# Optimization experiments

Measured on AMD Instinct MI355X. Metric: run time of the kernel, lower is better.

## Reference

```python
import jax, jax.numpy as jnp
import numpy as np

NUM_CLASSES = 81
NEG_RATIO = 3
POS_FRAC = 0.03  # realistic fraction of positive (matched) anchors


def setup_inputs() -> dict:
    key = jax.random.key(0)
    k1, k2, k3, k4, k5 = jax.random.split(key, 5)
    B, A, C = 64, 8732, NUM_CLASSES
    pred_loc = jax.random.normal(k1, (B, A, 4), dtype=jnp.float32)
    pred_conf = jax.random.normal(k2, (B, A, C), dtype=jnp.float32)
    gt_loc = jax.random.normal(k3, (B, A, 4), dtype=jnp.float32)
    raw_cls = jax.random.randint(k4, (B, A), 1, C)
    is_pos = jax.random.uniform(k5, (B, A)) < POS_FRAC
    gt_label = jnp.where(is_pos, raw_cls, 0).astype(jnp.int32)
    return {"pred_loc": pred_loc, "pred_conf": pred_conf, "gt_loc": gt_loc, "gt_label": gt_label}


def reference(pred_loc, pred_conf, gt_loc, gt_label):
    # pred_loc/gt_loc: [B, A, 4]; pred_conf: [B, A, C]; gt_label: [B, A] int
    pos = gt_label > 0  # [B, A]

    # Smooth L1 (beta=1), summed over positive anchors only (mask instead of boolean gather)
    d = jnp.abs(pred_loc - gt_loc)
    sl1 = jnp.where(d < 1.0, 0.5 * d * d, d - 0.5)
    loc_loss = jnp.sum(sl1 * pos[..., None].astype(sl1.dtype))

    # Per-anchor cross-entropy
    logp = jax.nn.log_softmax(pred_conf, axis=-1)  # [B, A, C]
    ce = -jnp.take_along_axis(logp, gt_label[..., None].astype(jnp.int32), axis=-1)[..., 0]  # [B, A]

    cef = ce.reshape(-1)
    posf = pos.reshape(-1)
    num_pos = jnp.sum(posf)
    num_neg = jnp.minimum(NEG_RATIO * num_pos, posf.size - num_pos)

    # Hard-negative mining: rank negatives by CE descending; select top num_neg.
    neg_vals = jnp.where(posf, -jnp.inf, cef)
    order = jnp.argsort(-neg_vals)  # indices sorted by descending negative loss
    rank = jnp.zeros_like(order).at[order].set(jnp.arange(order.size))
    neg_sel = (rank < num_neg) & (~posf)

    pos_conf_loss = jnp.sum(jnp.where(posf, cef, 0.0))
    neg_conf_loss = jnp.sum(jnp.where(neg_sel, cef, 0.0))

    total = (loc_loss + pos_conf_loss + neg_conf_loss) / num_pos.astype(cef.dtype)
    return total
```

## Files before the change

### kernel.cpp

```cpp
#include <hip/hip_runtime.h>
#include <hip/hip_bf16.h>
#include <math.h>

#define NB   64
#define NA   8732
#define NCLS 81
#define NTOT (NB * NA)
#define NTILE (NTOT / 16)
#define NSLICE 64
#define K1BLK  4096
#define SUMBLK 256

#define OFF_KEYS   0
#define OFF_HISTA  (NTOT * 4)
#define OFF_HIST2  (OFF_HISTA + NSLICE * 256 * 4)
#define OFF_SCAL   (OFF_HIST2 + 4096 * 4)
#define OFF_PBNP   (OFF_SCAL + 64)
#define OFF_PBPC   (OFF_PBNP + K1BLK * 4)
#define OFF_PBNEG  (OFF_PBPC + K1BLK * 4)
#define OFF_PBLOC  (OFF_PBNEG + SUMBLK * 4)
#define OFF_PBBIN  (OFF_PBLOC + SUMBLK * 4)
#define ZERO_BYTES (NSLICE * 256 * 4 + 4096 * 4 + 64)

__device__ __forceinline__ unsigned f2k(float f) {
  unsigned u = __float_as_uint(f);
  return (u & 0x80000000u) ? ~u : (u | 0x80000000u);
}
__device__ __forceinline__ float k2fv(unsigned u) {
  return __uint_as_float((u & 0x80000000u) ? (u ^ 0x80000000u) : ~u);
}

#define DPPF(v, ctrl) \
  __int_as_float(__builtin_amdgcn_update_dpp(0, __float_as_int(v), ctrl, 0xF, 0xF, true))

__global__ __launch_bounds__(256, 7) void mbl_k1(
    const float* __restrict__ pred_conf, const int* __restrict__ gt_label,
    unsigned* __restrict__ keys, unsigned* __restrict__ hista,
    unsigned* __restrict__ pb_np, float* __restrict__ pb_pc) {
  __shared__ float srow[4][1312];
  __shared__ unsigned lhist[256];
  __shared__ float s_pc[4];
  __shared__ unsigned s_np[4];
  lhist[threadIdx.x] = 0u;
  __syncthreads();

  const int lane = threadIdx.x & 63;
  const int wid  = threadIdx.x >> 6;
  const int gw   = (blockIdx.x << 2) + wid;
  const int l    = lane & 3;
  const int q    = lane >> 2;
  float* slice = srow[wid];
  float4* s4 = (float4*)slice;

  float posconf = 0.f;
  unsigned npos = 0u;

  for (int tile = gw; tile < NTILE; tile += K1BLK * 4) {
    const float4* src = (const float4*)pred_conf + (unsigned)tile * 324u;
    const float4 r0 = src[lane];
    const float4 r1 = src[lane + 64];
    const float4 r2 = src[lane + 128];
    const float4 r3 = src[lane + 192];
    const float4 r4 = src[lane + 256];
    float4 r5;
    if (lane < 4) r5 = src[lane + 320];
    const int lab = gt_label[(tile << 4) + q];

    s4[lane]       = r0;
    s4[lane + 64]  = r1;
    s4[lane + 128] = r2;
    s4[lane + 192] = r3;
    s4[lane + 256] = r4;
    if (lane < 4) s4[lane + 320] = r5;

    const int rb = q * 81;
    float e = 0.f;
#pragma unroll
    for (int j = 0; j < 20; ++j) e += __expf(slice[rb + l + 4 * j]);
    if (l == 0) e += __expf(slice[rb + 80]);
    e += DPPF(e, 0xB1);
    e += DPPF(e, 0x4E);
    const float pick = slice[rb + lab];

    if (l == 0) {
      const float ce = __logf(e) - pick;
      const int a = (tile << 4) + q;
      if (lab > 0) {
        npos += 1u; posconf += ce; keys[a] = 0u;
      } else {
        const unsigned u = f2k(ce);
        keys[a] = u;
        atomicAdd(&lhist[u >> 24], 1u);
      }
    }
  }

#pragma unroll
  for (int s = 1; s < 64; s <<= 1) {
    posconf += __shfl_xor(posconf, s);
    npos    += (unsigned)__shfl_xor((int)npos, s);
  }
  if ((threadIdx.x & 63) == 0) { s_pc[wid] = posconf; s_np[wid] = npos; }
  __syncthreads();
  if (threadIdx.x == 0) {
    pb_pc[blockIdx.x] = s_pc[0] + s_pc[1] + s_pc[2] + s_pc[3];
    pb_np[blockIdx.x] = s_np[0] + s_np[1] + s_np[2] + s_np[3];
  }
  const unsigned hv = lhist[threadIdx.x];
  if (hv) atomicAdd(&hista[(blockIdx.x & (NSLICE - 1)) * 256 + threadIdx.x], hv);
}

__global__ __launch_bounds__(256) void mbl_sel1(const unsigned* __restrict__ hista,
                                                const unsigned* __restrict__ pb_np,
                                                const float* __restrict__ pb_pc,
                                                unsigned* __restrict__ scal_u,
                                                float* __restrict__ scal_f) {
  __shared__ unsigned partial[256];
  __shared__ float q_pc[4];
  __shared__ unsigned q_np[4];
  __shared__ unsigned s_k;
  const int t = threadIdx.x;

  unsigned np = 0u; float pc = 0.f;
  for (int i = t; i < K1BLK; i += 256) { np += pb_np[i]; pc += pb_pc[i]; }
#pragma unroll
  for (int s = 1; s < 64; s <<= 1) {
    np += (unsigned)__shfl_xor((int)np, s);
    pc += __shfl_xor(pc, s);
  }
  if ((t & 63) == 0) { q_np[t >> 6] = np; q_pc[t >> 6] = pc; }
  __syncthreads();
  if (t == 0) {
    const unsigned tot = q_np[0] + q_np[1] + q_np[2] + q_np[3];
    scal_u[0] = tot;
    scal_f[2] = q_pc[0] + q_pc[1] + q_pc[2] + q_pc[3];
    const unsigned k = min(3u * tot, (unsigned)NTOT - tot);
    s_k = k; scal_u[4] = k;
    if (k == 0u) {
      scal_u[7] = 0xFFFFFFFFu; scal_u[8] = 0u;
      scal_u[9] = 0xFFFFFFFFu; scal_u[10] = 1u;
    }
  }
  __syncthreads();
  const unsigned k = s_k;
  if (k == 0u) return;

  unsigned s = 0u;
  for (int sl = 0; sl < NSLICE; ++sl) s += hista[sl * 256 + t];
  unsigned val = s;
  partial[t] = val;
  __syncthreads();
  for (int off = 1; off < 256; off <<= 1) {
    const unsigned add = (t + off < 256) ? partial[t + off] : 0u;
    __syncthreads();
    val += add;
    partial[t] = val;
    __syncthreads();
  }
  const unsigned suf = val - s;
  if (suf < k && k <= suf + s) { scal_u[5] = (unsigned)t; scal_u[6] = suf; }
}

__global__ __launch_bounds__(256) void mbl_h2(const unsigned* __restrict__ keys,
                                              unsigned* __restrict__ hist2,
                                              const unsigned* __restrict__ scal_u) {
  if (scal_u[4] == 0u) return;
  __shared__ unsigned lh[4096];
  for (int i = threadIdx.x; i < 4096; i += 256) lh[i] = 0u;
  __syncthreads();
  const unsigned b1 = scal_u[5];
  const int stride = gridDim.x * 256;
  for (int i = blockIdx.x * 256 + threadIdx.x; i < NTOT; i += stride) {
    const unsigned key = keys[i];
    if ((key >> 24) == b1) atomicAdd(&lh[(key >> 12) & 0xFFFu], 1u);
  }
  __syncthreads();
  for (int i = threadIdx.x; i < 4096; i += 256) {
    const unsigned v = lh[i];
    if (v) atomicAdd(&hist2[i], v);
  }
}

__global__ __launch_bounds__(1024) void mbl_sel2(const unsigned* __restrict__ hist2,
                                                 unsigned* __restrict__ scal_u) {
  __shared__ unsigned partial[1024];
  if (scal_u[4] == 0u) return;
  const unsigned kt = scal_u[4] - scal_u[6];
  const unsigned b1 = scal_u[5];
  const int t = threadIdx.x;
  unsigned s = 0u;
#pragma unroll
  for (int i = 0; i < 4; ++i) s += hist2[t * 4 + i];
  unsigned val = s;
  partial[t] = val;
  __syncthreads();
  for (int off = 1; off < 1024; off <<= 1) {
    const unsigned add = (t + off < 1024) ? partial[t + off] : 0u;
    __syncthreads();
    val += add;
    partial[t] = val;
    __syncthreads();
  }
  const unsigned suf = val - s;
  if (suf < kt && kt <= suf + s) {
    unsigned c = suf;
    for (int b = 3; b >= 0; --b) {
      const unsigned h = hist2[t * 4 + b];
      if (c + h >= kt) {
        const unsigned bin = (unsigned)(t * 4 + b);
        scal_u[7] = (b1 << 24) | (bin << 12) | 0xFFFu;
        scal_u[9] = (b1 << 12) | bin;
        scal_u[8] = kt - c;
        scal_u[10] = h;
        break;
      }
      c += h;
    }
  }
}

__global__ __launch_bounds__(256) void mbl_sum(
    const unsigned* __restrict__ keys, const int* __restrict__ gt_label,
    const float* __restrict__ pred_loc, const float* __restrict__ gt_loc,
    const unsigned* __restrict__ scal_u,
    float* __restrict__ pb_neg, float* __restrict__ pb_loc,
    float* __restrict__ pb_bin) {
  __shared__ float q_n[4], q_l[4], q_b[4];
  const unsigned T = scal_u[7];
  const unsigned P20 = scal_u[9];
  float acc = 0.f, lacc = 0.f, bacc = 0.f;
  const int stride = gridDim.x * 256;
  for (int i = blockIdx.x * 256 + threadIdx.x; i < NTOT; i += stride) {
    const unsigned key = keys[i];
    if (key > T) acc += k2fv(key);
    else if ((key >> 12) == P20) bacc += k2fv(key);
    const int lb = gt_label[i];
    if (lb > 0) {
      const float4 pl = ((const float4*)pred_loc)[i];
      const float4 gl = ((const float4*)gt_loc)[i];
      float d;
      d = fabsf(pl.x - gl.x); lacc += (d < 1.f) ? 0.5f * d * d : d - 0.5f;
      d = fabsf(pl.y - gl.y); lacc += (d < 1.f) ? 0.5f * d * d : d - 0.5f;
      d = fabsf(pl.z - gl.z); lacc += (d < 1.f) ? 0.5f * d * d : d - 0.5f;
      d = fabsf(pl.w - gl.w); lacc += (d < 1.f) ? 0.5f * d * d : d - 0.5f;
    }
  }
#pragma unroll
  for (int s = 1; s < 64; s <<= 1) {
    acc  += __shfl_xor(acc, s);
    lacc += __shfl_xor(lacc, s);
    bacc += __shfl_xor(bacc, s);
  }
  const int wv = threadIdx.x >> 6;
  if ((threadIdx.x & 63) == 0) { q_n[wv] = acc; q_l[wv] = lacc; q_b[wv] = bacc; }
  __syncthreads();
  if (threadIdx.x == 0) {
    pb_neg[blockIdx.x] = q_n[0] + q_n[1] + q_n[2] + q_n[3];
    pb_loc[blockIdx.x] = q_l[0] + q_l[1] + q_l[2] + q_l[3];
    pb_bin[blockIdx.x] = q_b[0] + q_b[1] + q_b[2] + q_b[3];
  }
}

__global__ __launch_bounds__(256) void mbl_fin(const unsigned* __restrict__ scal_u,
                                               const float* __restrict__ scal_f,
                                               const float* __restrict__ pb_neg,
                                               const float* __restrict__ pb_loc,
                                               const float* __restrict__ pb_bin,
                                               float* __restrict__ out) {
  __shared__ float q_n[4], q_l[4], q_b[4];
  const int t = threadIdx.x;
  float n = pb_neg[t], l = pb_loc[t], b = pb_bin[t];
#pragma unroll
  for (int s = 1; s < 64; s <<= 1) {
    n += __shfl_xor(n, s);
    l += __shfl_xor(l, s);
    b += __shfl_xor(b, s);
  }
  const int wv = t >> 6;
  if ((t & 63) == 0) { q_n[wv] = n; q_l[wv] = l; q_b[wv] = b; }
  __syncthreads();
  if (t == 0) {
    float negsum = q_n[0] + q_n[1] + q_n[2] + q_n[3];
    const float locsum = q_l[0] + q_l[1] + q_l[2] + q_l[3];
    const float binsum = q_b[0] + q_b[1] + q_b[2] + q_b[3];
    const unsigned r = scal_u[8];
    if (r > 0u) negsum += (float)r * (binsum / (float)scal_u[10]);
    out[0] = (locsum + scal_f[2] + negsum) / (float)scal_u[0];
  }
}

extern "C" void kernel_launch(void* const* d_in, const int* in_sizes, int n_in,
                              void* d_out, int out_size, void* d_ws, size_t ws_size,
                              hipStream_t stream) {
  const float* pred_loc  = (const float*)d_in[0];
  const float* pred_conf = (const float*)d_in[1];
  const float* gt_loc    = (const float*)d_in[2];
  const int*   gt_label  = (const int*)d_in[3];
  float* out = (float*)d_out;

  char* ws = (char*)d_ws;
  unsigned* keys   = (unsigned*)(ws + OFF_KEYS);
  unsigned* hista  = (unsigned*)(ws + OFF_HISTA);
  unsigned* hist2  = (unsigned*)(ws + OFF_HIST2);
  unsigned* scal_u = (unsigned*)(ws + OFF_SCAL);
  float*    scal_f = (float*)(ws + OFF_SCAL);
  unsigned* pb_np  = (unsigned*)(ws + OFF_PBNP);
  float*    pb_pc  = (float*)(ws + OFF_PBPC);
  float*    pb_neg = (float*)(ws + OFF_PBNEG);
  float*    pb_loc = (float*)(ws + OFF_PBLOC);
  float*    pb_bin = (float*)(ws + OFF_PBBIN);

  hipMemsetAsync(ws + OFF_HISTA, 0, ZERO_BYTES, stream);

  mbl_k1<<<K1BLK, 256, 0, stream>>>(pred_conf, gt_label, keys, hista, pb_np, pb_pc);
  mbl_sel1<<<1, 256, 0, stream>>>(hista, pb_np, pb_pc, scal_u, scal_f);
  mbl_h2<<<256, 256, 0, stream>>>(keys, hist2, scal_u);
  mbl_sel2<<<1, 1024, 0, stream>>>(hist2, scal_u);
  mbl_sum<<<SUMBLK, 256, 0, stream>>>(keys, gt_label, pred_loc, gt_loc, scal_u,
                                      pb_neg, pb_loc, pb_bin);
  mbl_fin<<<1, 256, 0, stream>>>(scal_u, scal_f, pb_neg, pb_loc, pb_bin, out);
}
```

Measured before the change: 69.98 us.

## Fuse selection stages into histogram and sum kernels to cut launches

Merges the single-block threshold selections into the kernels that follow them. Every block of the second-histogram kernel redundantly reduces the per-block counts and scans the coarse histogram. Every block of the sum kernel redundantly scans the fine histogram. The final reduction is folded in through a last-block atomic ticket. This removes three kernel launches and their serialization gaps, at the cost of redundant per-block scan work and a threadfence/atomic tail.

```diff
diff --git a/kernel.cpp b/kernel.cpp
--- a/kernel.cpp
+++ b/kernel.cpp
@@ -9,18 +9,20 @@
 #define NTILE (NTOT / 16)
 #define NSLICE 64
 #define K1BLK  4096
+#define T1BLK  256
 #define SUMBLK 256
 
 #define OFF_KEYS   0
 #define OFF_HISTA  (NTOT * 4)
 #define OFF_HIST2  (OFF_HISTA + NSLICE * 256 * 4)
 #define OFF_SCAL   (OFF_HIST2 + 4096 * 4)
-#define OFF_PBNP   (OFF_SCAL + 64)
+#define OFF_TICK   (OFF_SCAL + 64)
+#define OFF_PBNP   (OFF_TICK + 64)
 #define OFF_PBPC   (OFF_PBNP + K1BLK * 4)
 #define OFF_PBNEG  (OFF_PBPC + K1BLK * 4)
 #define OFF_PBLOC  (OFF_PBNEG + SUMBLK * 4)
 #define OFF_PBBIN  (OFF_PBLOC + SUMBLK * 4)
-#define ZERO_BYTES (NSLICE * 256 * 4 + 4096 * 4 + 64)
+#define ZERO_BYTES (NSLICE * 256 * 4 + 4096 * 4 + 64 + 64)
 
 __device__ __forceinline__ unsigned f2k(float f) {
   unsigned u = __float_as_uint(f);
@@ -110,15 +112,16 @@
   if (hv) atomicAdd(&hista[(blockIdx.x & (NSLICE - 1)) * 256 + threadIdx.x], hv);
 }
 
-__global__ __launch_bounds__(256) void mbl_sel1(const unsigned* __restrict__ hista,
-                                                const unsigned* __restrict__ pb_np,
-                                                const float* __restrict__ pb_pc,
-                                                unsigned* __restrict__ scal_u,
-                                                float* __restrict__ scal_f) {
+__global__ __launch_bounds__(256) void mbl_t1(
+    const unsigned* __restrict__ keys, const unsigned* __restrict__ hista,
+    const unsigned* __restrict__ pb_np, const float* __restrict__ pb_pc,
+    unsigned* __restrict__ hist2,
+    unsigned* __restrict__ scal_u, float* __restrict__ scal_f) {
+  __shared__ unsigned lh[4096];
   __shared__ unsigned partial[256];
   __shared__ float q_pc[4];
   __shared__ unsigned q_np[4];
-  __shared__ unsigned s_k;
+  __shared__ unsigned s_k, s_b1, s_cnt;
   const int t = threadIdx.x;
 
   unsigned np = 0u; float pc = 0.f;
@@ -132,13 +135,12 @@
   __syncthreads();
   if (t == 0) {
     const unsigned tot = q_np[0] + q_np[1] + q_np[2] + q_np[3];
-    scal_u[0] = tot;
-    scal_f[2] = q_pc[0] + q_pc[1] + q_pc[2] + q_pc[3];
     const unsigned k = min(3u * tot, (unsigned)NTOT - tot);
-    s_k = k; scal_u[4] = k;
-    if (k == 0u) {
-      scal_u[7] = 0xFFFFFFFFu; scal_u[8] = 0u;
-      scal_u[9] = 0xFFFFFFFFu; scal_u[10] = 1u;
+    s_k = k;
+    if (blockIdx.x == 0) {
+      scal_u[0] = tot;
+      scal_f[2] = q_pc[0] + q_pc[1] + q_pc[2] + q_pc[3];
+      scal_u[4] = k;
     }
   }
   __syncthreads();
@@ -158,79 +160,82 @@
     __syncthreads();
   }
   const unsigned suf = val - s;
-  if (suf < k && k <= suf + s) { scal_u[5] = (unsigned)t; scal_u[6] = suf; }
-}
-
-__global__ __launch_bounds__(256) void mbl_h2(const unsigned* __restrict__ keys,
-                                              unsigned* __restrict__ hist2,
-                                              const unsigned* __restrict__ scal_u) {
-  if (scal_u[4] == 0u) return;
-  __shared__ unsigned lh[4096];
-  for (int i = threadIdx.x; i < 4096; i += 256) lh[i] = 0u;
-  __syncthreads();
-  const unsigned b1 = scal_u[5];
+  if (suf < k && k <= suf + s) { s_b1 = (unsigned)t; s_cnt = suf; }
+  __syncthreads();
+  const unsigned b1 = s_b1;
+  if (blockIdx.x == 0 && t == 0) { scal_u[5] = b1; scal_u[6] = s_cnt; }
+
+  for (int i = t; i < 4096; i += 256) lh[i] = 0u;
+  __syncthreads();
   const int stride = gridDim.x * 256;
-  for (int i = blockIdx.x * 256 + threadIdx.x; i < NTOT; i += stride) {
+  for (int i = blockIdx.x * 256 + t; i < NTOT; i += stride) {
     const unsigned key = keys[i];
     if ((key >> 24) == b1) atomicAdd(&lh[(key >> 12) & 0xFFFu], 1u);
   }
   __syncthreads();
-  for (int i = threadIdx.x; i < 4096; i += 256) {
+  for (int i = t; i < 4096; i += 256) {
     const unsigned v = lh[i];
     if (v) atomicAdd(&hist2[i], v);
   }
 }
 
-__global__ __launch_bounds__(1024) void mbl_sel2(const unsigned* __restrict__ hist2,
-                                                 unsigned* __restrict__ scal_u) {
-  __shared__ unsigned partial[1024];
-  if (scal_u[4] == 0u) return;
-  const unsigned kt = scal_u[4] - scal_u[6];
-  const unsigned b1 = scal_u[5];
+__global__ __launch_bounds__(256) void mbl_t2(
+    const unsigned* __restrict__ keys, const int* __restrict__ gt_label,
+    const float* __restrict__ pred_loc, const float* __restrict__ gt_loc,
+    const unsigned* __restrict__ hist2,
+    const unsigned* __restrict__ scal_u, const float* __restrict__ scal_f,
+    float* __restrict__ pb_neg, float* __restrict__ pb_loc,
+    float* __restrict__ pb_bin, unsigned* __restrict__ tick,
+    float* __restrict__ out) {
+  __shared__ unsigned partial[256];
+  __shared__ float q_n[4], q_l[4], q_b[4];
+  __shared__ unsigned s_T, s_P20, s_r, s_bt;
+  __shared__ bool s_last;
   const int t = threadIdx.x;
-  unsigned s = 0u;
-#pragma unroll
-  for (int i = 0; i < 4; ++i) s += hist2[t * 4 + i];
-  unsigned val = s;
-  partial[t] = val;
-  __syncthreads();
-  for (int off = 1; off < 1024; off <<= 1) {
-    const unsigned add = (t + off < 1024) ? partial[t + off] : 0u;
-    __syncthreads();
-    val += add;
+  const unsigned k = scal_u[4];
+
+  unsigned T, P20, r, bt;
+  if (k == 0u) {
+    T = 0xFFFFFFFFu; P20 = 0xFFFFFFFFu; r = 0u; bt = 1u;
+  } else {
+    const unsigned b1 = scal_u[5];
+    const unsigned kt = k - scal_u[6];
+    unsigned s = 0u;
+#pragma unroll
+    for (int i = 0; i < 16; ++i) s += hist2[t * 16 + i];
+    unsigned val = s;
     partial[t] = val;
     __syncthreads();
-  }
-  const unsigned suf = val - s;
-  if (suf < kt && kt <= suf + s) {
-    unsigned c = suf;
-    for (int b = 3; b >= 0; --b) {
-      const unsigned h = hist2[t * 4 + b];
-      if (c + h >= kt) {
-        const unsigned bin = (unsigned)(t * 4 + b);
-        scal_u[7] = (b1 << 24) | (bin << 12) | 0xFFFu;
-        scal_u[9] = (b1 << 12) | bin;
-        scal_u[8] = kt - c;
-        scal_u[10] = h;
-        break;
+    for (int off = 1; off < 256; off <<= 1) {
+      const unsigned add = (t + off < 256) ? partial[t + off] : 0u;
+      __syncthreads();
+      val += add;
+      partial[t] = val;
+      __syncthreads();
+    }
+    const unsigned suf = val - s;
+    if (suf < kt && kt <= suf + s) {
+      unsigned c = suf;
+      for (int b = 15; b >= 0; --b) {
+        const unsigned h = hist2[t * 16 + b];
+        if (c + h >= kt) {
+          const unsigned bin = (unsigned)(t * 16 + b);
+          s_T = (b1 << 24) | (bin << 12) | 0xFFFu;
+          s_P20 = (b1 << 12) | bin;
+          s_r = kt - c;
+          s_bt = h;
+          break;
+        }
+        c += h;
       }
-      c += h;
-    }
-  }
-}
-
-__global__ __launch_bounds__(256) void mbl_sum(
-    const unsigned* __restrict__ keys, const int* __restrict__ gt_label,
-    const float* __restrict__ pred_loc, const float* __restrict__ gt_loc,
-    const unsigned* __restrict__ scal_u,
-    float* __restrict__ pb_neg, float* __restrict__ pb_loc,
-    float* __restrict__ pb_bin) {
-  __shared__ float q_n[4], q_l[4], q_b[4];
-  const unsigned T = scal_u[7];
-  const unsigned P20 = scal_u[9];
+    }
+    __syncthreads();
+    T = s_T; P20 = s_P20; r = s_r; bt = s_bt;
+  }
+
   float acc = 0.f, lacc = 0.f, bacc = 0.f;
   const int stride = gridDim.x * 256;
-  for (int i = blockIdx.x * 256 + threadIdx.x; i < NTOT; i += stride) {
+  for (int i = blockIdx.x * 256 + t; i < NTOT; i += stride) {
     const unsigned key = keys[i];
     if (key > T) acc += k2fv(key);
     else if ((key >> 12) == P20) bacc += k2fv(key);
@@ -251,40 +256,36 @@
     lacc += __shfl_xor(lacc, s);
     bacc += __shfl_xor(bacc, s);
   }
-  const int wv = threadIdx.x >> 6;
-  if ((threadIdx.x & 63) == 0) { q_n[wv] = acc; q_l[wv] = lacc; q_b[wv] = bacc; }
-  __syncthreads();
-  if (threadIdx.x == 0) {
+  const int wv = t >> 6;
+  if ((t & 63) == 0) { q_n[wv] = acc; q_l[wv] = lacc; q_b[wv] = bacc; }
+  __syncthreads();
+  if (t == 0) {
     pb_neg[blockIdx.x] = q_n[0] + q_n[1] + q_n[2] + q_n[3];
     pb_loc[blockIdx.x] = q_l[0] + q_l[1] + q_l[2] + q_l[3];
     pb_bin[blockIdx.x] = q_b[0] + q_b[1] + q_b[2] + q_b[3];
   }
-}
-
-__global__ __launch_bounds__(256) void mbl_fin(const unsigned* __restrict__ scal_u,
-                                               const float* __restrict__ scal_f,
-                                               const float* __restrict__ pb_neg,
-                                               const float* __restrict__ pb_loc,
-                                               const float* __restrict__ pb_bin,
-                                               float* __restrict__ out) {
-  __shared__ float q_n[4], q_l[4], q_b[4];
-  const int t = threadIdx.x;
-  float n = pb_neg[t], l = pb_loc[t], b = pb_bin[t];
+
+  __threadfence();
+  if (t == 0) s_last = (atomicAdd(&tick[0], 1u) == (unsigned)(gridDim.x - 1));
+  __syncthreads();
+  if (!s_last) return;
+  __threadfence();
+
+  float n = pb_neg[t], l2 = pb_loc[t], b2 = pb_bin[t];
 #pragma unroll
   for (int s = 1; s < 64; s <<= 1) {
-    n += __shfl_xor(n, s);
-    l += __shfl_xor(l, s);
-    b += __shfl_xor(b, s);
-  }
-  const int wv = t >> 6;
-  if ((t & 63) == 0) { q_n[wv] = n; q_l[wv] = l; q_b[wv] = b; }
+    n  += __shfl_xor(n, s);
+    l2 += __shfl_xor(l2, s);
+    b2 += __shfl_xor(b2, s);
+  }
+  __syncthreads();
+  if ((t & 63) == 0) { q_n[wv] = n; q_l[wv] = l2; q_b[wv] = b2; }
   __syncthreads();
   if (t == 0) {
     float negsum = q_n[0] + q_n[1] + q_n[2] + q_n[3];
     const float locsum = q_l[0] + q_l[1] + q_l[2] + q_l[3];
     const float binsum = q_b[0] + q_b[1] + q_b[2] + q_b[3];
-    const unsigned r = scal_u[8];
-    if (r > 0u) negsum += (float)r * (binsum / (float)scal_u[10]);
+    if (r > 0u) negsum += (float)r * (binsum / (float)bt);
     out[0] = (locsum + scal_f[2] + negsum) / (float)scal_u[0];
   }
 }
@@ -304,6 +305,7 @@
   unsigned* hist2  = (unsigned*)(ws + OFF_HIST2);
   unsigned* scal_u = (unsigned*)(ws + OFF_SCAL);
   float*    scal_f = (float*)(ws + OFF_SCAL);
+  unsigned* tick   = (unsigned*)(ws + OFF_TICK);
   unsigned* pb_np  = (unsigned*)(ws + OFF_PBNP);
   float*    pb_pc  = (float*)(ws + OFF_PBPC);
   float*    pb_neg = (float*)(ws + OFF_PBNEG);
@@ -313,10 +315,8 @@
   hipMemsetAsync(ws + OFF_HISTA, 0, ZERO_BYTES, stream);
 
   mbl_k1<<<K1BLK, 256, 0, stream>>>(pred_conf, gt_label, keys, hista, pb_np, pb_pc);
-  mbl_sel1<<<1, 256, 0, stream>>>(hista, pb_np, pb_pc, scal_u, scal_f);
-  mbl_h2<<<256, 256, 0, stream>>>(keys, hist2, scal_u);
-  mbl_sel2<<<1, 1024, 0, stream>>>(hist2, scal_u);
-  mbl_sum<<<SUMBLK, 256, 0, stream>>>(keys, gt_label, pred_loc, gt_loc, scal_u,
-                                      pb_neg, pb_loc, pb_bin);
-  mbl_fin<<<1, 256, 0, stream>>>(scal_u, scal_f, pb_neg, pb_loc, pb_bin, out);
-}
+  mbl_t1<<<T1BLK, 256, 0, stream>>>(keys, hista, pb_np, pb_pc, hist2, scal_u, scal_f);
+  mbl_t2<<<SUMBLK, 256, 0, stream>>>(keys, gt_label, pred_loc, gt_loc, hist2,
+                                     scal_u, scal_f, pb_neg, pb_loc, pb_bin,
+                                     tick, out);
+}
```

Result: slower. 86.64 us (+23.8%).

## Replace two-pass radix select with single fixed-width linear histogram over CE values

Applied to the files above, without the earlier changes.

Replaces the two-level radix histogram over bit-packed float keys with one 2048-bin linear histogram of cross-entropy values scaled by 64, fused into the first kernel. This removes the second histogram pass over all keys and one selection kernel. The threshold bin's partial contribution is approximated by its average, now over much wider bins (1/64 width), so accuracy depends on the CE value distribution and clamping at the top bin. Larger shared-memory histogram lowers k1 occupancy hint to 5.

```diff
diff --git a/kernel.cpp b/kernel.cpp
--- a/kernel.cpp
+++ b/kernel.cpp
@@ -7,41 +7,34 @@
 #define NCLS 81
 #define NTOT (NB * NA)
 #define NTILE (NTOT / 16)
-#define NSLICE 64
+#define NBIN  2048
+#define CSCALE 64.0f
+#define NSLICE 16
 #define K1BLK  4096
 #define SUMBLK 256
 
 #define OFF_KEYS   0
 #define OFF_HISTA  (NTOT * 4)
-#define OFF_HIST2  (OFF_HISTA + NSLICE * 256 * 4)
-#define OFF_SCAL   (OFF_HIST2 + 4096 * 4)
+#define OFF_SCAL   (OFF_HISTA + NSLICE * NBIN * 4)
 #define OFF_PBNP   (OFF_SCAL + 64)
 #define OFF_PBPC   (OFF_PBNP + K1BLK * 4)
 #define OFF_PBNEG  (OFF_PBPC + K1BLK * 4)
 #define OFF_PBLOC  (OFF_PBNEG + SUMBLK * 4)
 #define OFF_PBBIN  (OFF_PBLOC + SUMBLK * 4)
-#define ZERO_BYTES (NSLICE * 256 * 4 + 4096 * 4 + 64)
-
-__device__ __forceinline__ unsigned f2k(float f) {
-  unsigned u = __float_as_uint(f);
-  return (u & 0x80000000u) ? ~u : (u | 0x80000000u);
-}
-__device__ __forceinline__ float k2fv(unsigned u) {
-  return __uint_as_float((u & 0x80000000u) ? (u ^ 0x80000000u) : ~u);
-}
+#define ZERO_BYTES (NSLICE * NBIN * 4 + 64)
 
 #define DPPF(v, ctrl) \
   __int_as_float(__builtin_amdgcn_update_dpp(0, __float_as_int(v), ctrl, 0xF, 0xF, true))
 
-__global__ __launch_bounds__(256, 7) void mbl_k1(
+__global__ __launch_bounds__(256, 5) void mbl_k1(
     const float* __restrict__ pred_conf, const int* __restrict__ gt_label,
-    unsigned* __restrict__ keys, unsigned* __restrict__ hista,
+    float* __restrict__ keys, unsigned* __restrict__ hista,
     unsigned* __restrict__ pb_np, float* __restrict__ pb_pc) {
   __shared__ float srow[4][1312];
-  __shared__ unsigned lhist[256];
+  __shared__ unsigned lhist[NBIN];
   __shared__ float s_pc[4];
   __shared__ unsigned s_np[4];
-  lhist[threadIdx.x] = 0u;
+  for (int i = threadIdx.x; i < NBIN; i += 256) lhist[i] = 0u;
   __syncthreads();
 
   const int lane = threadIdx.x & 63;
@@ -86,11 +79,12 @@
       const float ce = __logf(e) - pick;
       const int a = (tile << 4) + q;
       if (lab > 0) {
-        npos += 1u; posconf += ce; keys[a] = 0u;
+        npos += 1u; posconf += ce; keys[a] = -1.f;
       } else {
-        const unsigned u = f2k(ce);
-        keys[a] = u;
-        atomicAdd(&lhist[u >> 24], 1u);
+        keys[a] = ce;
+        int bin = (int)(ce * CSCALE);
+        bin = min(bin, NBIN - 1);
+        atomicAdd(&lhist[bin], 1u);
       }
     }
   }
@@ -106,15 +100,19 @@
     pb_pc[blockIdx.x] = s_pc[0] + s_pc[1] + s_pc[2] + s_pc[3];
     pb_np[blockIdx.x] = s_np[0] + s_np[1] + s_np[2] + s_np[3];
   }
-  const unsigned hv = lhist[threadIdx.x];
-  if (hv) atomicAdd(&hista[(blockIdx.x & (NSLICE - 1)) * 256 + threadIdx.x], hv);
-}
-
-__global__ __launch_bounds__(256) void mbl_sel1(const unsigned* __restrict__ hista,
-                                                const unsigned* __restrict__ pb_np,
-                                                const float* __restrict__ pb_pc,
-                                                unsigned* __restrict__ scal_u,
-                                                float* __restrict__ scal_f) {
+  const unsigned slice_off = (blockIdx.x & (NSLICE - 1)) * NBIN;
+  for (int i = threadIdx.x; i < NBIN; i += 256) {
+    const unsigned v = lhist[i];
+    if (v) atomicAdd(&hista[slice_off + i], v);
+  }
+}
+
+__global__ __launch_bounds__(256) void mbl_sel(const unsigned* __restrict__ hista,
+                                               const unsigned* __restrict__ pb_np,
+                                               const float* __restrict__ pb_pc,
+                                               unsigned* __restrict__ scal_u,
+                                               float* __restrict__ scal_f) {
+  __shared__ unsigned hbin[NBIN];
   __shared__ unsigned partial[256];
   __shared__ float q_pc[4];
   __shared__ unsigned q_np[4];
@@ -136,17 +134,21 @@
     scal_f[2] = q_pc[0] + q_pc[1] + q_pc[2] + q_pc[3];
     const unsigned k = min(3u * tot, (unsigned)NTOT - tot);
     s_k = k; scal_u[4] = k;
-    if (k == 0u) {
-      scal_u[7] = 0xFFFFFFFFu; scal_u[8] = 0u;
-      scal_u[9] = 0xFFFFFFFFu; scal_u[10] = 1u;
-    }
+    if (k == 0u) { scal_u[5] = NBIN; scal_u[6] = 0u; scal_u[7] = 1u; }
   }
   __syncthreads();
   const unsigned k = s_k;
   if (k == 0u) return;
 
   unsigned s = 0u;
-  for (int sl = 0; sl < NSLICE; ++sl) s += hista[sl * 256 + t];
+#pragma unroll
+  for (int j = 0; j < 8; ++j) {
+    unsigned v = 0u;
+#pragma unroll
+    for (int sl = 0; sl < NSLICE; ++sl) v += hista[sl * NBIN + t * 8 + j];
+    hbin[t * 8 + j] = v;
+    s += v;
+  }
   unsigned val = s;
   partial[t] = val;
   __syncthreads();
@@ -158,82 +160,39 @@
     __syncthreads();
   }
   const unsigned suf = val - s;
-  if (suf < k && k <= suf + s) { scal_u[5] = (unsigned)t; scal_u[6] = suf; }
-}
-
-__global__ __launch_bounds__(256) void mbl_h2(const unsigned* __restrict__ keys,
-                                              unsigned* __restrict__ hist2,
-                                              const unsigned* __restrict__ scal_u) {
-  if (scal_u[4] == 0u) return;
-  __shared__ unsigned lh[4096];
-  for (int i = threadIdx.x; i < 4096; i += 256) lh[i] = 0u;
-  __syncthreads();
-  const unsigned b1 = scal_u[5];
-  const int stride = gridDim.x * 256;
-  for (int i = blockIdx.x * 256 + threadIdx.x; i < NTOT; i += stride) {
-    const unsigned key = keys[i];
-    if ((key >> 24) == b1) atomicAdd(&lh[(key >> 12) & 0xFFFu], 1u);
-  }
-  __syncthreads();
-  for (int i = threadIdx.x; i < 4096; i += 256) {
-    const unsigned v = lh[i];
-    if (v) atomicAdd(&hist2[i], v);
-  }
-}
-
-__global__ __launch_bounds__(1024) void mbl_sel2(const unsigned* __restrict__ hist2,
-                                                 unsigned* __restrict__ scal_u) {
-  __shared__ unsigned partial[1024];
-  if (scal_u[4] == 0u) return;
-  const unsigned kt = scal_u[4] - scal_u[6];
-  const unsigned b1 = scal_u[5];
-  const int t = threadIdx.x;
-  unsigned s = 0u;
-#pragma unroll
-  for (int i = 0; i < 4; ++i) s += hist2[t * 4 + i];
-  unsigned val = s;
-  partial[t] = val;
-  __syncthreads();
-  for (int off = 1; off < 1024; off <<= 1) {
-    const unsigned add = (t + off < 1024) ? partial[t + off] : 0u;
-    __syncthreads();
-    val += add;
-    partial[t] = val;
-    __syncthreads();
-  }
-  const unsigned suf = val - s;
-  if (suf < kt && kt <= suf + s) {
+  if (suf < k && k <= suf + s) {
     unsigned c = suf;
-    for (int b = 3; b >= 0; --b) {
-      const unsigned h = hist2[t * 4 + b];
-      if (c + h >= kt) {
-        const unsigned bin = (unsigned)(t * 4 + b);
-        scal_u[7] = (b1 << 24) | (bin << 12) | 0xFFFu;
-        scal_u[9] = (b1 << 12) | bin;
-        scal_u[8] = kt - c;
-        scal_u[10] = h;
+    for (int b = 7; b >= 0; --b) {
+      const unsigned hb = hbin[t * 8 + b];
+      if (c + hb >= k) {
+        scal_u[5] = (unsigned)(t * 8 + b);
+        scal_u[6] = k - c;
+        scal_u[7] = hb;
         break;
       }
-      c += h;
+      c += hb;
     }
   }
 }
 
 __global__ __launch_bounds__(256) void mbl_sum(
-    const unsigned* __restrict__ keys, const int* __restrict__ gt_label,
+    const float* __restrict__ keys, const int* __restrict__ gt_label,
     const float* __restrict__ pred_loc, const float* __restrict__ gt_loc,
     const unsigned* __restrict__ scal_u,
     float* __restrict__ pb_neg, float* __restrict__ pb_loc,
     float* __restrict__ pb_bin) {
   __shared__ float q_n[4], q_l[4], q_b[4];
-  const unsigned T = scal_u[7];
-  const unsigned P20 = scal_u[9];
+  const int bstar = (int)scal_u[5];
   float acc = 0.f, lacc = 0.f, bacc = 0.f;
   const int stride = gridDim.x * 256;
   for (int i = blockIdx.x * 256 + threadIdx.x; i < NTOT; i += stride) {
-    const unsigned key = keys[i];
-    if (key > T) acc += k2fv(key);
-    else if ((key >> 12) == P20) bacc += k2fv(key);
+    const float kf = keys[i];
+    if (kf >= 0.f) {
+      int b = (int)(kf * CSCALE);
+      b = min(b, NBIN - 1);
+      if (b > bstar) acc += kf;
+      else if (b == bstar) bacc += kf;
+    }
     const int lb = gt_label[i];
     if (lb > 0) {
       const float4 pl = ((const float4*)pred_loc)[i];
@@ -283,8 +242,8 @@
     float negsum = q_n[0] + q_n[1] + q_n[2] + q_n[3];
     const float locsum = q_l[0] + q_l[1] + q_l[2] + q_l[3];
     const float binsum = q_b[0] + q_b[1] + q_b[2] + q_b[3];
-    const unsigned r = scal_u[8];
-    if (r > 0u) negsum += (float)r * (binsum / (float)scal_u[10]);
+    const unsigned r = scal_u[6];
+    if (r > 0u) negsum += (float)r * (binsum / (float)scal_u[7]);
     out[0] = (locsum + scal_f[2] + negsum) / (float)scal_u[0];
   }
 }
@@ -299,9 +258,8 @@
   float* out = (float*)d_out;
 
   char* ws = (char*)d_ws;
-  unsigned* keys   = (unsigned*)(ws + OFF_KEYS);
+  float*    keys   = (float*)(ws + OFF_KEYS);
   unsigned* hista  = (unsigned*)(ws + OFF_HISTA);
-  unsigned* hist2  = (unsigned*)(ws + OFF_HIST2);
   unsigned* scal_u = (unsigned*)(ws + OFF_SCAL);
   float*    scal_f = (float*)(ws + OFF_SCAL);
   unsigned* pb_np  = (unsigned*)(ws + OFF_PBNP);
@@ -313,9 +271,7 @@
   hipMemsetAsync(ws + OFF_HISTA, 0, ZERO_BYTES, stream);
 
   mbl_k1<<<K1BLK, 256, 0, stream>>>(pred_conf, gt_label, keys, hista, pb_np, pb_pc);
-  mbl_sel1<<<1, 256, 0, stream>>>(hista, pb_np, pb_pc, scal_u, scal_f);
-  mbl_h2<<<256, 256, 0, stream>>>(keys, hist2, scal_u);
-  mbl_sel2<<<1, 1024, 0, stream>>>(hist2, scal_u);
+  mbl_sel<<<1, 256, 0, stream>>>(hista, pb_np, pb_pc, scal_u, scal_f);
   mbl_sum<<<SUMBLK, 256, 0, stream>>>(keys, gt_label, pred_loc, gt_loc, scal_u,
                                       pb_neg, pb_loc, pb_bin);
   mbl_fin<<<1, 256, 0, stream>>>(scal_u, scal_f, pb_neg, pb_loc, pb_bin, out);
```

After: 70.48 us. Within noise of the previous version (+0.7%).
